# Performance work log

Measured on AMD Instinct MI355X. Metric: run time of the kernel, lower is better.

Reference implementation:

```python
import jax, jax.numpy as jnp
import numpy as np

N_NODES = 4096
IN_FEATURES = 256
N_HEADS = 8
N_HIDDEN = 32  # out_features // n_heads = 256 // 8
NEG_SLOPE = 0.2
MASK_FILL = -1e9


def setup_inputs() -> dict:
    key = jax.random.key(0)
    k_h, k_adj, k_w, k_a = jax.random.split(key, 4)
    h = jax.random.normal(k_h, (N_NODES, IN_FEATURES), dtype=jnp.float32)
    adj_mat = jax.random.randint(k_adj, (N_NODES, N_NODES, 1), 0, 2, dtype=jnp.int32)
    # linear: Linear(in_features, n_hidden*n_heads, bias=False) -> W: [in, H*F]
    W = jax.random.normal(k_w, (IN_FEATURES, N_HEADS * N_HIDDEN), dtype=jnp.float32) / np.sqrt(IN_FEATURES)
    # attn: Linear(2*n_hidden, 1, bias=False) -> a: [2*F]
    a = jax.random.normal(k_a, (2 * N_HIDDEN,), dtype=jnp.float32) / np.sqrt(2 * N_HIDDEN)
    return {"h": h, "adj_mat": adj_mat, "W": W, "a": a}


def reference(h, adj_mat, W, a):
    n = h.shape[0]
    # g: [n, H, F]
    g = (h @ W).reshape(n, N_HEADS, N_HIDDEN)
    # attn(concat(g_i, g_j)) == g_i . a[:F] + g_j . a[F:]  (decomposed, same math,
    # avoids materializing the O(N^2 * H * 2F) concat tensor of the torch code)
    a_src, a_dst = a[:N_HIDDEN], a[N_HIDDEN:]
    s_src = jnp.einsum('nhf,f->nh', g, a_src)  # [n, H]
    s_dst = jnp.einsum('nhf,f->nh', g, a_dst)  # [n, H]
    e = jax.nn.leaky_relu(s_src[:, None, :] + s_dst[None, :, :], negative_slope=NEG_SLOPE)  # [n, n, H]
    e = jnp.where(adj_mat == 0, MASK_FILL, e)  # adj_mat [n, n, 1] broadcasts over heads
    att = jax.nn.softmax(e, axis=1)  # softmax over source nodes j (dropout in eval mode = identity)
    out = jnp.einsum('ijh,jhf->ihf', att, g)  # [n, H, F]
    return out.reshape(n, N_HEADS * N_HIDDEN)  # is_concat=True
```

## Files before the change

kernel.cpp:

```cpp
#include <hip/hip_runtime.h>

#define NN 4096
#define FIN 256
#define CC 256
#define NH 8
#define NW32 (NN / 32)

typedef __attribute__((ext_vector_type(8))) short short8;
typedef __attribute__((ext_vector_type(4))) float f32x4;
typedef __attribute__((ext_vector_type(4))) unsigned int u32x4;

__device__ __forceinline__ unsigned cvtpk_bf16(float lo, float hi) {
  unsigned r;
  asm("v_cvt_pk_bf16_f32 %0, %1, %2" : "=v"(r) : "v"(lo), "v"(hi));
  return r;
}

__device__ __forceinline__ unsigned short bf16rn(float x) {
  unsigned int u = __builtin_bit_cast(unsigned int, x);
  u += 0x7fffu + ((u >> 16) & 1u);
  return (unsigned short)(u >> 16);
}

__device__ __forceinline__ void gl_lds16(const void* g, void* l) {
  __builtin_amdgcn_global_load_lds(
      (const __attribute__((address_space(1))) void*)g,
      (__attribute__((address_space(3))) void*)l, 16, 0, 0);
}

#define GROWS 8
#define GEMM_BLKS (NN / GROWS)
#define BP_BLKS (NN * NW32 / 256)
__global__ __launch_bounds__(256) void k_gemm(
    const float* __restrict__ h, const float* __restrict__ W,
    const float* __restrict__ a, const int* __restrict__ adj,
    unsigned int* __restrict__ adjb, unsigned short* __restrict__ gTs,
    float4* __restrict__ spack, float* __restrict__ dtc) {
  __shared__ float hs[GROWS][FIN];
  const int t = threadIdx.x;
  const int bx = blockIdx.x;

  if (bx >= GEMM_BLKS) {
    const int wid = (bx - GEMM_BLKS) * 256 + t;
    const int row = wid >> 7, wd = wid & 127;
    const int* src = adj + (size_t)row * NN + wd * 32;
    int4 v[8];
#pragma unroll
    for (int s = 0; s < 8; ++s) v[s] = *(const int4*)&src[s * 4];
    unsigned int bits = 0;
#pragma unroll
    for (int s = 0; s < 8; ++s) {
      bits |= (v[s].x ? 1u : 0u) << (s * 4 + 0);
      bits |= (v[s].y ? 1u : 0u) << (s * 4 + 1);
      bits |= (v[s].z ? 1u : 0u) << (s * 4 + 2);
      bits |= (v[s].w ? 1u : 0u) << (s * 4 + 3);
    }
    adjb[(size_t)row * NW32 + wd] = bits;
    return;
  }

  const int r0 = bx * GROWS;
#pragma unroll
  for (int idx = t; idx < GROWS * FIN / 4; idx += 256) {
    const int r = idx >> 6, c4 = idx & 63;
    *(float4*)&hs[r][c4 * 4] =
        *(const float4*)&h[(size_t)(r0 + r) * FIN + c4 * 4];
  }
  __syncthreads();
  const int c = t;
  float acc[GROWS];
#pragma unroll
  for (int r = 0; r < GROWS; ++r) acc[r] = 0.f;
  for (int k = 0; k < FIN; k += 4) {
    const float w0 = W[(size_t)(k + 0) * CC + c];
    const float w1 = W[(size_t)(k + 1) * CC + c];
    const float w2 = W[(size_t)(k + 2) * CC + c];
    const float w3 = W[(size_t)(k + 3) * CC + c];
#pragma unroll
    for (int r = 0; r < GROWS; ++r) {
      const float4 hv = *(const float4*)&hs[r][k];
      acc[r] += hv.x * w0 + hv.y * w1 + hv.z * w2 + hv.w * w3;
    }
  }
  const int f = c & 31, hh = c >> 5;
  const float aS = a[f], aD = a[32 + f];
  unsigned short gu[GROWS];
#pragma unroll
  for (int r = 0; r < GROWS; ++r) {
    float ps = acc[r] * aS, pd = acc[r] * aD;
#pragma unroll
    for (int m = 1; m < 32; m <<= 1) {
      ps += __shfl_xor(ps, m, 64);
      pd += __shfl_xor(pd, m, 64);
    }
    if (f == 0) {
      const int n = r0 + r;
      spack[(size_t)hh * NN + n] =
          make_float4(__expf(ps), __expf(0.2f * ps), 0.f, 0.f);
      float* dc = dtc + (size_t)(n >> 5) * 512 + hh * 32 + (n & 31);
      dc[0] = __expf(pd);
      dc[256] = __expf(0.2f * pd);
    }
    gu[r] = bf16rn(acc[r]);
  }
  uint4 gv;
  gv.x = (unsigned)gu[0] | ((unsigned)gu[1] << 16);
  gv.y = (unsigned)gu[2] | ((unsigned)gu[3] << 16);
  gv.z = (unsigned)gu[4] | ((unsigned)gu[5] << 16);
  gv.w = (unsigned)gu[6] | ((unsigned)gu[7] << 16);
  const int jc = r0 >> 5, qq = (r0 >> 3) & 3;
  const int p = qq ^ ((c >> 1) & 3);
  *(uint4*)(gTs + ((size_t)jc * 1024 + c * 4 + p) * 8) = gv;
}

struct Buf {
  unsigned short gt[2][8192];
  float dt[2][2][NH][32];
};

__global__ __launch_bounds__(256, 2) void k_attn(
    const unsigned int* __restrict__ adjb, const unsigned short* __restrict__ gTs,
    const float4* __restrict__ spack, const float* __restrict__ dtc,
    float* __restrict__ acc_ws, float* __restrict__ l_ws,
    float* __restrict__ out, const int splits, const int direct) {
  __shared__ Buf buf[2];

  const int lane = threadIdx.x & 63;
  const int w = threadIdx.x >> 6;
  const int il = lane & 15, q = lane >> 4;
  const int bx = blockIdx.x;
  const int sp = bx & (splits - 1);
  const int ib = bx / splits;
  const int i0w = ib * 64 + (w >> 1) * 32;
  const int hquad = w & 1;
  const int jrange = NN / splits, j0b = sp * jrange;
  const int c0 = j0b >> 5;

  float e1v[4][2], e2v[4][2];
#pragma unroll
  for (int hp = 0; hp < 4; ++hp)
#pragma unroll
    for (int it = 0; it < 2; ++it) {
      const float4 v =
          spack[(size_t)(hquad * 4 + hp) * NN + i0w + it * 16 + il];
      e1v[hp][it] = v.x; e2v[hp][it] = v.y;
    }

  f32x4 acc[4][2][2];
  f32x4 lac[4][2];
#pragma unroll
  for (int hp = 0; hp < 4; ++hp)
#pragma unroll
    for (int it = 0; it < 2; ++it) {
#pragma unroll
      for (int r = 0; r < 4; ++r) lac[hp][it][r] = 0.f;
#pragma unroll
      for (int ft = 0; ft < 2; ++ft)
#pragma unroll
        for (int r = 0; r < 4; ++r) acc[hp][it][ft][r] = 0.f;
    }

  const short8 ones = {(short)0x3F80, (short)0x3F80, (short)0x3F80,
                       (short)0x3F80, (short)0x3F80, (short)0x3F80,
                       (short)0x3F80, (short)0x3F80};

  const unsigned long long* ab0 =
      (const unsigned long long*)(adjb + (size_t)(i0w + il) * NW32) +
      (j0b >> 6);
  const unsigned long long* ab1 =
      (const unsigned long long*)(adjb + (size_t)(i0w + 16 + il) * NW32) +
      (j0b >> 6);
  const int sh = q * 8;
  const int pswz = q ^ ((il >> 1) & 3);

  auto stage = [&](Buf* b, int jb) {
    const unsigned short* src = gTs + (size_t)(c0 + jb * 2) * 8192;
#pragma unroll
    for (int pass = 0; pass < 8; ++pass) {
      const int base = pass * 256 + w * 64;
      gl_lds16(src + (size_t)(base + lane) * 8, (char*)&b->gt[0][0] + base * 16);
    }
    const float* dsrc = dtc + (size_t)(c0 + jb * 2) * 512;
    gl_lds16(dsrc + (size_t)(w * 64 + lane) * 4,
             (char*)&b->dt[0][0][0][0] + (w * 64) * 16);
  };

  const int nbuf = jrange / 64;
  stage(&buf[0], 0);
  unsigned long long pb0 = ab0[0], pb1 = ab1[0];
  __syncthreads();
  int cur = 0;

  for (int jb = 0; jb < nbuf; ++jb) {
    if (jb + 1 < nbuf) stage(&buf[cur ^ 1], jb + 1);
    const Buf* bc = &buf[cur];
    const unsigned int bl0[2] = {(unsigned int)pb0, (unsigned int)(pb0 >> 32)};
    const unsigned int bl1[2] = {(unsigned int)pb1, (unsigned int)(pb1 >> 32)};
    if (jb + 1 < nbuf) { pb0 = ab0[jb + 1]; pb1 = ab1[jb + 1]; }

#pragma unroll
    for (int sub = 0; sub < 2; ++sub) {
      float adf[2][8];
#pragma unroll
      for (int e = 0; e < 8; ++e) {
        adf[0][e] = (float)((bl0[sub] >> (sh + e)) & 1u);
        adf[1][e] = (float)((bl1[sub] >> (sh + e)) & 1u);
      }
#pragma unroll
      for (int hp = 0; hp < 4; ++hp) {
        const int hh = hquad * 4 + hp;
        float e1j[8], e2j[8];
        *(float4*)&e1j[0] = *(const float4*)&bc->dt[sub][0][hh][q * 8];
        *(float4*)&e1j[4] = *(const float4*)&bc->dt[sub][0][hh][q * 8 + 4];
        *(float4*)&e2j[0] = *(const float4*)&bc->dt[sub][1][hh][q * 8];
        *(float4*)&e2j[4] = *(const float4*)&bc->dt[sub][1][hh][q * 8 + 4];
        const int u0 = (hh * 32 + il) * 4 + pswz;
        const short8 b0 = *(const short8*)&bc->gt[sub][u0 * 8];
        const short8 b1 = *(const short8*)&bc->gt[sub][(u0 + 64) * 8];
#pragma unroll
        for (int it = 0; it < 2; ++it) {
          const float ei1 = e1v[hp][it], ei2 = e2v[hp][it];
          float wv[8];
#pragma unroll
          for (int e = 0; e < 8; ++e)
            wv[e] = fmaxf(ei1 * e1j[e], ei2 * e2j[e]) * adf[it][e];
          u32x4 uu;
#pragma unroll
          for (int m = 0; m < 4; ++m)
            uu[m] = cvtpk_bf16(wv[2 * m], wv[2 * m + 1]);
          const short8 afr = __builtin_bit_cast(short8, uu);
          acc[hp][it][0] = __builtin_amdgcn_mfma_f32_16x16x32_bf16(
              afr, b0, acc[hp][it][0], 0, 0, 0);
          acc[hp][it][1] = __builtin_amdgcn_mfma_f32_16x16x32_bf16(
              afr, b1, acc[hp][it][1], 0, 0, 0);
          lac[hp][it] = __builtin_amdgcn_mfma_f32_16x16x32_bf16(
              afr, ones, lac[hp][it], 0, 0, 0);
        }
      }
    }
    __syncthreads();
    cur ^= 1;
  }

  if (direct) {
#pragma unroll
    for (int hp = 0; hp < 4; ++hp) {
      const int hh = hquad * 4 + hp;
#pragma unroll
      for (int it = 0; it < 2; ++it)
#pragma unroll
        for (int r = 0; r < 4; ++r) {
          const float inv = 1.f / lac[hp][it][r];
          const size_t irow = i0w + it * 16 + q * 4 + r;
#pragma unroll
          for (int ft = 0; ft < 2; ++ft)
            out[irow * CC + hh * 32 + ft * 16 + il] =
                acc[hp][it][ft][r] * inv;
        }
    }
  } else {
#pragma unroll
    for (int hp = 0; hp < 4; ++hp) {
      const int hh = hquad * 4 + hp;
#pragma unroll
      for (int it = 0; it < 2; ++it)
#pragma unroll
        for (int r = 0; r < 4; ++r) {
          const size_t irow = i0w + it * 16 + q * 4 + r;
          if (il == 0)
            l_ws[((size_t)sp * NH + hh) * NN + irow] = lac[hp][it][r];
#pragma unroll
          for (int ft = 0; ft < 2; ++ft)
            acc_ws[((size_t)sp * NN + irow) * CC + hh * 32 + ft * 16 + il] =
                acc[hp][it][ft][r];
        }
    }
  }
}

__global__ __launch_bounds__(256) void k_combine(
    const float* __restrict__ acc_ws, const float* __restrict__ l_ws,
    float* __restrict__ out, const int splits) {
  const int idx = blockIdx.x * 256 + threadIdx.x;
  const int row = idx >> 6, c4 = idx & 63;
  const int hh = c4 >> 3;
  float ax = 0.f, ay = 0.f, az = 0.f, aw = 0.f, l = 0.f;
  for (int s = 0; s < splits; ++s) {
    const float4 v =
        *(const float4*)&acc_ws[((size_t)s * NN + row) * CC + c4 * 4];
    ax += v.x; ay += v.y; az += v.z; aw += v.w;
    l += l_ws[((size_t)s * NH + hh) * NN + row];
  }
  const float inv = 1.f / l;
  *(float4*)&out[(size_t)row * CC + c4 * 4] =
      make_float4(ax * inv, ay * inv, az * inv, aw * inv);
}

extern "C" void kernel_launch(void* const* d_in, const int* in_sizes, int n_in,
                              void* d_out, int out_size, void* d_ws,
                              size_t ws_size, hipStream_t stream) {
  (void)in_sizes; (void)n_in; (void)out_size;
  const float* h = (const float*)d_in[0];
  const int* adj = (const int*)d_in[1];
  const float* W = (const float*)d_in[2];
  const float* a = (const float*)d_in[3];
  float* out = (float*)d_out;
  char* ws = (char*)d_ws;

  unsigned short* gTs = (unsigned short*)ws;
  float4* spack = (float4*)(ws + (size_t)NN * CC * 2);
  float* dtc = (float*)(spack + (size_t)NH * NN);
  unsigned int* adjb =
      (unsigned int*)(dtc + (size_t)(NN / 32) * 512);
  char* after = (char*)(adjb + (size_t)NN * NW32);
  const size_t base = (size_t)(after - ws);
  const size_t per_split = (size_t)NN * CC * 4 + (size_t)NH * NN * 4;

  int splits = 1;
  if (ws_size >= base + 8 * per_split) splits = 8;
  else if (ws_size >= base + 4 * per_split) splits = 4;
  else if (ws_size >= base + 2 * per_split) splits = 2;

  k_gemm<<<GEMM_BLKS + BP_BLKS, 256, 0, stream>>>(h, W, a, adj, adjb, gTs,
                                                  spack, dtc);

  const int nblk = (NN / 64) * splits;
  if (splits == 1) {
    k_attn<<<nblk, 256, 0, stream>>>(adjb, gTs, spack, dtc, nullptr, nullptr,
                                     out, 1, 1);
  } else {
    float* acc_ws = (float*)after;
    float* l_ws = acc_ws + (size_t)splits * NN * CC;
    k_attn<<<nblk, 256, 0, stream>>>(adjb, gTs, spack, dtc, acc_ws, l_ws, out,
                                     splits, 0);
    k_combine<<<NN * CC / 4 / 256, 256, 0, stream>>>(acc_ws, l_ws, out,
                                                     splits);
  }
}
```

Baseline: 72.40 us.

## Split attention blocks by head group instead of by row halves

Each attention block now covers 128 destination rows and 2 heads (4 head groups), where before it covered 64 rows and all 8 heads. The dtc layout is changed so each block stages only its heads' source-side exponentials and g columns. This shrinks per-block LDS staging and accumulator registers, which should allow more occupancy and less wasted global-to-LDS traffic. In exchange, the adjacency bitmask is now reread once per head group, and grid size and block indexing change.

```diff
diff --git a/kernel.cpp b/kernel.cpp
--- a/kernel.cpp
+++ b/kernel.cpp
@@ -97,9 +97,9 @@
       const int n = r0 + r;
       spack[(size_t)hh * NN + n] =
           make_float4(__expf(ps), __expf(0.2f * ps), 0.f, 0.f);
-      float* dc = dtc + (size_t)(n >> 5) * 512 + hh * 32 + (n & 31);
+      float* dc = dtc + ((size_t)(n >> 5) * NH + hh) * 64 + (n & 31);
       dc[0] = __expf(pd);
-      dc[256] = __expf(0.2f * pd);
+      dc[32] = __expf(0.2f * pd);
     }
     gu[r] = bf16rn(acc[r]);
   }
@@ -114,8 +114,8 @@
 }
 
 struct Buf {
-  unsigned short gt[2][8192];
-  float dt[2][2][NH][32];
+  unsigned short gt[2][2048];
+  float dt[2][2][2][32];
 };
 
 __global__ __launch_bounds__(256, 2) void k_attn(
@@ -130,26 +130,26 @@
   const int il = lane & 15, q = lane >> 4;
   const int bx = blockIdx.x;
   const int sp = bx & (splits - 1);
-  const int ib = bx / splits;
-  const int i0w = ib * 64 + (w >> 1) * 32;
-  const int hquad = w & 1;
+  const int rest = bx / splits;
+  const int hg = rest & 3;
+  const int ib = rest >> 2;
+  const int i0w = ib * 128 + w * 32;
   const int jrange = NN / splits, j0b = sp * jrange;
   const int c0 = j0b >> 5;
 
-  float e1v[4][2], e2v[4][2];
-#pragma unroll
-  for (int hp = 0; hp < 4; ++hp)
+  float e1v[2][2], e2v[2][2];
+#pragma unroll
+  for (int hp = 0; hp < 2; ++hp)
 #pragma unroll
     for (int it = 0; it < 2; ++it) {
-      const float4 v =
-          spack[(size_t)(hquad * 4 + hp) * NN + i0w + it * 16 + il];
+      const float4 v = spack[(size_t)(hg * 2 + hp) * NN + i0w + it * 16 + il];
       e1v[hp][it] = v.x; e2v[hp][it] = v.y;
     }
 
-  f32x4 acc[4][2][2];
-  f32x4 lac[4][2];
-#pragma unroll
-  for (int hp = 0; hp < 4; ++hp)
+  f32x4 acc[2][2][2];
+  f32x4 lac[2][2];
+#pragma unroll
+  for (int hp = 0; hp < 2; ++hp)
 #pragma unroll
     for (int it = 0; it < 2; ++it) {
 #pragma unroll
@@ -174,15 +174,20 @@
   const int pswz = q ^ ((il >> 1) & 3);
 
   auto stage = [&](Buf* b, int jb) {
-    const unsigned short* src = gTs + (size_t)(c0 + jb * 2) * 8192;
-#pragma unroll
-    for (int pass = 0; pass < 8; ++pass) {
-      const int base = pass * 256 + w * 64;
-      gl_lds16(src + (size_t)(base + lane) * 8, (char*)&b->gt[0][0] + base * 16);
-    }
-    const float* dsrc = dtc + (size_t)(c0 + jb * 2) * 512;
-    gl_lds16(dsrc + (size_t)(w * 64 + lane) * 4,
-             (char*)&b->dt[0][0][0][0] + (w * 64) * 16);
+#pragma unroll
+    for (int sub = 0; sub < 2; ++sub) {
+      const unsigned short* src =
+          gTs + ((size_t)(c0 + jb * 2 + sub) * 1024 + hg * 256 + w * 64) * 8;
+      gl_lds16(src + (size_t)lane * 8, (char*)&b->gt[sub][0] + (w * 64) * 16);
+    }
+    if (w == 0) {
+      const float* dsrc =
+          dtc +
+          ((size_t)(c0 + jb * 2 + (lane >> 5)) * NH + hg * 2 + ((lane >> 4) & 1)) *
+              64 +
+          ((lane >> 3) & 1) * 32 + (lane & 7) * 4;
+      gl_lds16(dsrc, (char*)&b->dt[0][0][0][0]);
+    }
   };
 
   const int nbuf = jrange / 64;
@@ -207,14 +212,13 @@
         adf[1][e] = (float)((bl1[sub] >> (sh + e)) & 1u);
       }
 #pragma unroll
-      for (int hp = 0; hp < 4; ++hp) {
-        const int hh = hquad * 4 + hp;
+      for (int hp = 0; hp < 2; ++hp) {
         float e1j[8], e2j[8];
-        *(float4*)&e1j[0] = *(const float4*)&bc->dt[sub][0][hh][q * 8];
-        *(float4*)&e1j[4] = *(const float4*)&bc->dt[sub][0][hh][q * 8 + 4];
-        *(float4*)&e2j[0] = *(const float4*)&bc->dt[sub][1][hh][q * 8];
-        *(float4*)&e2j[4] = *(const float4*)&bc->dt[sub][1][hh][q * 8 + 4];
-        const int u0 = (hh * 32 + il) * 4 + pswz;
+        *(float4*)&e1j[0] = *(const float4*)&bc->dt[sub][hp][0][q * 8];
+        *(float4*)&e1j[4] = *(const float4*)&bc->dt[sub][hp][0][q * 8 + 4];
+        *(float4*)&e2j[0] = *(const float4*)&bc->dt[sub][hp][1][q * 8];
+        *(float4*)&e2j[4] = *(const float4*)&bc->dt[sub][hp][1][q * 8 + 4];
+        const int u0 = (hp * 32 + il) * 4 + pswz;
         const short8 b0 = *(const short8*)&bc->gt[sub][u0 * 8];
         const short8 b1 = *(const short8*)&bc->gt[sub][(u0 + 64) * 8];
 #pragma unroll
@@ -244,8 +248,8 @@
 
   if (direct) {
 #pragma unroll
-    for (int hp = 0; hp < 4; ++hp) {
-      const int hh = hquad * 4 + hp;
+    for (int hp = 0; hp < 2; ++hp) {
+      const int hh = hg * 2 + hp;
 #pragma unroll
       for (int it = 0; it < 2; ++it)
 #pragma unroll
@@ -260,8 +264,8 @@
     }
   } else {
 #pragma unroll
-    for (int hp = 0; hp < 4; ++hp) {
-      const int hh = hquad * 4 + hp;
+    for (int hp = 0; hp < 2; ++hp) {
+      const int hh = hg * 2 + hp;
 #pragma unroll
       for (int it = 0; it < 2; ++it)
 #pragma unroll
@@ -311,7 +315,7 @@
   float4* spack = (float4*)(ws + (size_t)NN * CC * 2);
   float* dtc = (float*)(spack + (size_t)NH * NN);
   unsigned int* adjb =
-      (unsigned int*)(dtc + (size_t)(NN / 32) * 512);
+      (unsigned int*)(dtc + (size_t)(NN / 32) * NH * 64);
   char* after = (char*)(adjb + (size_t)NN * NW32);
   const size_t base = (size_t)(after - ws);
   const size_t per_split = (size_t)NN * CC * 4 + (size_t)NH * NN * 4;
@@ -324,7 +328,7 @@
   k_gemm<<<GEMM_BLKS + BP_BLKS, 256, 0, stream>>>(h, W, a, adj, adjb, gTs,
                                                   spack, dtc);
 
-  const int nblk = (NN / 64) * splits;
+  const int nblk = (NN / 128) * 4 * splits;
   if (splits == 1) {
     k_attn<<<nblk, 256, 0, stream>>>(adjb, gTs, spack, dtc, nullptr, nullptr,
                                      out, 1, 1);
```

New measurement: 69.73 us. -3.7%, faster.
